# Kernel tuning notes

Measured on AMD Instinct MI355X. Metric: run time of the kernel, lower is better.

Reference implementation:

```python
import math
import jax, jax.numpy as jnp
import numpy as np

THETA = 10000.0

def _rope_rotate(x, pos):
    # x: [N,H,T,d] with d even; pos: [T] (int or float positions)
    d = x.shape[-1]
    freqs = THETA ** (-jnp.arange(0, d, 2, dtype=jnp.float32) / d)      # [d/2]
    ang = pos.astype(jnp.float32)[:, None] * freqs                       # [T, d/2]
    cos, sin = jnp.cos(ang), jnp.sin(ang)                                # broadcast over N,H
    x1, x2 = x[..., 0::2], x[..., 1::2]                                  # interleaved pairs
    r1 = x1 * cos - x2 * sin
    r2 = x1 * sin + x2 * cos
    return jnp.stack([r1, r2], axis=-1).reshape(x.shape)

def _apply_rope_2d(q, k, pos_h, pos_w):
    # axial 2D RoPE: first half of head_dim rotated by pos_h, second half by pos_w
    dh = q.shape[-1]
    half = dh // 2
    q = jnp.concatenate([_rope_rotate(q[..., :half], pos_h),
                         _rope_rotate(q[..., half:], pos_w)], axis=-1)
    k = jnp.concatenate([_rope_rotate(k[..., :half], pos_h),
                         _rope_rotate(k[..., half:], pos_w)], axis=-1)
    return q, k

def setup_inputs() -> dict:
    key = jax.random.key(0)
    ks = jax.random.split(key, 6)
    N, T, D, H = 4, 2048, 512, 8
    GH, GW = 64, 32  # 64x32 token grid, GH*GW == T
    x = jax.random.normal(ks[0], (N, T, D), dtype=jnp.float32)
    idx = jnp.arange(T, dtype=jnp.int32)
    pos_h = idx // GW
    pos_w = idx % GW
    scale_in = 1.0 / math.sqrt(D)
    w_qkv = jax.random.normal(ks[1], (D, 3 * D), dtype=jnp.float32) * scale_in
    w_proj = jax.random.normal(ks[2], (D, D), dtype=jnp.float32) * scale_in
    b_proj = jnp.zeros((D,), dtype=jnp.float32)
    return {"x": x, "pos_h": pos_h, "pos_w": pos_w,
            "w_qkv": w_qkv, "w_proj": w_proj, "b_proj": b_proj}

def reference(x, pos_h, pos_w, w_qkv, w_proj, b_proj):
    N, T, D = x.shape
    H = 8
    Dh = D // H
    qkv = x @ w_qkv                                   # [N,T,3D]
    q, k, v = jnp.split(qkv, 3, axis=-1)
    def to_heads(t):
        return t.reshape(N, T, H, Dh).transpose(0, 2, 1, 3)  # [N,H,T,Dh]
    q, k, v = to_heads(q), to_heads(k), to_heads(v)
    q, k = _apply_rope_2d(q, k, pos_h, pos_w)
    attn = jnp.einsum('nhtd,nhsd->nhts', q, k) * (1.0 / math.sqrt(Dh))  # [N,H,T,T]
    p = jax.nn.softmax(attn, axis=-1)
    o = jnp.einsum('nhts,nhsd->nhtd', p, v)           # [N,H,T,Dh]
    o = o.transpose(0, 2, 1, 3).reshape(N, T, D)
    return o @ w_proj + b_proj
```

## Files before the change

kernel.cpp:

```cpp
#include <hip/hip_runtime.h>

typedef __attribute__((ext_vector_type(4))) float f32x4;
typedef __attribute__((ext_vector_type(8))) _Float16 f16x8;
typedef __attribute__((ext_vector_type(2))) __fp16 fp16x2_raw;
typedef __attribute__((ext_vector_type(4))) unsigned int u32x4;
typedef __attribute__((ext_vector_type(2))) unsigned int u32x2;

#define MFMA_F16(a, b, c) __builtin_amdgcn_mfma_f32_16x16x32_f16((a), (b), (c), 0, 0, 0)

__device__ __forceinline__ unsigned int pkrtz(float a, float b) {
  union { fp16x2_raw h; unsigned int u; } v;
  v.h = __builtin_amdgcn_cvt_pkrtz(a, b);
  return v.u;
}

__device__ __forceinline__ float fexp2(float x) {
#if __has_builtin(__builtin_amdgcn_exp2f)
  return __builtin_amdgcn_exp2f(x);
#else
  float r;
  asm("v_exp_f32 %0, %1" : "=v"(r) : "v"(x));
  return r;
#endif
}
__device__ __forceinline__ float fsin_rev(float x) {
#if __has_builtin(__builtin_amdgcn_sinf)
  return __builtin_amdgcn_sinf(x);
#else
  float r; asm("v_sin_f32 %0, %1" : "=v"(r) : "v"(x)); return r;
#endif
}
__device__ __forceinline__ float fcos_rev(float x) {
#if __has_builtin(__builtin_amdgcn_cosf)
  return __builtin_amdgcn_cosf(x);
#else
  float r; asm("v_cos_f32 %0, %1" : "=v"(r) : "v"(x)); return r;
#endif
}

typedef const __attribute__((address_space(1))) unsigned int ga_u32_t;
typedef __attribute__((address_space(3))) unsigned int ls_u32_t;
__device__ __forceinline__ void gload16(const void* g, void* l) {
  __builtin_amdgcn_global_load_lds((ga_u32_t*)g, (ls_u32_t*)l, 16, 0, 0);
}

__device__ __forceinline__ void inv_swz64(int seg, int lane, int& r, int& ch) {
  int r_hi = seg * 8 + (lane >> 3);
  int r0 = ((lane >> 2) & 1) ^ ((r_hi >> 1) & 1);
  r = (r_hi << 1) | r0;
  ch = (lane & 3) ^ (r & 3);
}

__global__ __launch_bounds__(256)
void k_prep(const float* __restrict__ x, _Float16* __restrict__ xh,
            const float* __restrict__ wq, _Float16* __restrict__ wqT,
            const float* __restrict__ wp, _Float16* __restrict__ wpT) {
  const int b = blockIdx.x;
  const int tid = threadIdx.x;
  if (b < 4096) {
    int i = (b * 256 + tid) * 4;
    f32x4 v = *(const f32x4*)(x + i);
    u32x2 p;
    p.x = pkrtz(v[0], v[1]);
    p.y = pkrtz(v[2], v[3]);
    *(u32x2*)(xh + i) = p;
    return;
  }
  __shared__ float t[64][65];
  const int wb = b - 4096;
  const int bx = wb & 31, by = wb >> 5;
  const float* in = (bx < 24) ? wq : wp;
  _Float16* out = (bx < 24) ? wqT : wpT;
  const int N = (bx < 24) ? 1536 : 512;
  const int bn = ((bx < 24) ? bx : bx - 24) * 64, bk = by * 64;
  #pragma unroll
  for (int it = 0; it < 16; ++it) {
    int idx = it * 256 + tid;
    int kk = idx >> 6, nn = idx & 63;
    t[kk][nn] = in[(bk + kk) * N + bn + nn];
  }
  __syncthreads();
  #pragma unroll
  for (int it = 0; it < 16; ++it) {
    int idx = it * 256 + tid;
    int nn = idx >> 6, kk = idx & 63;
    out[(bn + nn) * 512 + bk + kk] = (_Float16)t[kk][nn];
  }
}

__global__ __launch_bounds__(256, 3)
void k_gemm_qkv(const _Float16* __restrict__ xh,
                const _Float16* __restrict__ wT,
                const int* __restrict__ pos_h,
                const int* __restrict__ pos_w,
                _Float16* __restrict__ qh,
                _Float16* __restrict__ kh,
                _Float16* __restrict__ vT) {
  __shared__ char As[8192], Bs[8192];
  const int tid = threadIdx.x;
  const int lane = tid & 63, w = tid >> 6;
  const int lr = lane & 15, g = lane >> 4;
  const int m0 = blockIdx.y * 128;
  const int n0 = blockIdx.x * 128;
  const int wr = w >> 1, wc = w & 1;

  const _Float16* asrc[2];
  const _Float16* bsrc[2];
  #pragma unroll
  for (int c = 0; c < 2; ++c) {
    int seg = w * 2 + c, r, ch;
    inv_swz64(seg, lane, r, ch);
    asrc[c] = xh + (size_t)(m0 + r) * 512 + ch * 8;
    bsrc[c] = wT + (size_t)(n0 + r) * 512 + ch * 8;
  }

  f32x4 acc[4][4];
  #pragma unroll
  for (int i = 0; i < 4; ++i)
    #pragma unroll
    for (int j = 0; j < 4; ++j) acc[i][j] = (f32x4){0.f, 0.f, 0.f, 0.f};

  for (int kt = 0; kt < 16; ++kt) {
    const int k0 = kt * 32;
    __syncthreads();
    #pragma unroll
    for (int c = 0; c < 2; ++c) {
      gload16(asrc[c] + k0, As + (w * 2 + c) * 1024);
      gload16(bsrc[c] + k0, Bs + (w * 2 + c) * 1024);
    }
    __syncthreads();

    f16x8 af[4], bf[4];
    #pragma unroll
    for (int mi = 0; mi < 4; ++mi) {
      int r = 64 * wr + 16 * mi + lr;
      af[mi] = *(const f16x8*)(As + (((r << 6) + (g << 4)) ^ ((r & 7) << 4)));
    }
    #pragma unroll
    for (int nj = 0; nj < 4; ++nj) {
      int r = 64 * wc + 16 * nj + lr;
      bf[nj] = *(const f16x8*)(Bs + (((r << 6) + (g << 4)) ^ ((r & 7) << 4)));
    }
    __builtin_amdgcn_s_setprio(1);
    #pragma unroll
    for (int mi = 0; mi < 4; ++mi)
      #pragma unroll
      for (int nj = 0; nj < 4; ++nj)
        acc[mi][nj] = MFMA_F16(af[mi], bf[nj], acc[mi][nj]);
    __builtin_amdgcn_s_setprio(0);
  }

  #pragma unroll
  for (int mi = 0; mi < 4; ++mi) {
    const int r0f = m0 + 64 * wr + 16 * mi + 4 * g;
    const int n = r0f >> 11;
    const int t = r0f & 2047;
    #pragma unroll
    for (int nj = 0; nj < 4; ++nj) {
      const int c = n0 + 64 * wc + 16 * nj + lr;
      const int mat = c >> 9;
      const int hh = (c >> 6) & 7;
      const int dh = c & 63;
      f32x4 v = acc[mi][nj];
      if (mat == 2) {
        int tperm = (t & ~31) + 8 * ((t >> 2) & 3) + 4 * ((t >> 4) & 1);
        u32x2 pk2;
        pk2.x = pkrtz(v[0], v[1]);
        pk2.y = pkrtz(v[2], v[3]);
        *(u32x2*)(vT + (size_t)((n * 8 + hh) * 64 + dh) * 2048 + tperm) = pk2;
      } else {
        const int p = (dh & 31) >> 1;
        const float freq_rev = fexp2((float)p * -0.8304820237218405f) * 0.15915494309189535f;
        const int odd = lane & 1;
        const int* posArr = (dh < 32) ? pos_h : pos_w;
        _Float16* dst = mat ? kh : qh;
        const float scale = mat ? 1.0f : 0.125f * 1.44269504088896f;
        #pragma unroll
        for (int i = 0; i < 4; ++i) {
          float val = v[i];
          float oth = __shfl_xor(val, 1);
          float ar = (float)posArr[t + i] * freq_rev;
          ar = ar - floorf(ar);
          float sv = fsin_rev(ar);
          float cv = fcos_rev(ar);
          float x1 = odd ? oth : val;
          float x2 = odd ? val : oth;
          float res = odd ? (x1 * sv + x2 * cv) : (x1 * cv - x2 * sv);
          dst[(size_t)((n * 8 + hh) * 2048 + t + i) * 64 + dh] = (_Float16)(res * scale);
        }
      }
    }
  }
}

__global__ __launch_bounds__(256, 3)
void k_attn(const _Float16* __restrict__ qh,
            const _Float16* __restrict__ kh,
            const _Float16* __restrict__ vp,
            _Float16* __restrict__ o_flat) {
  __shared__ char Ks[2][16384];
  __shared__ char Vs[16384];
  const int tid = threadIdx.x, lane = tid & 63, w = tid >> 6;
  const int lr = lane & 15, g = lane >> 4;
  const int bid = blockIdx.x;
  const int qt = (bid >> 3) & 15;
  const int nh = (bid & 7) + 8 * (bid >> 7);

  f16x8 qf[2][2];
  const _Float16* qbase = qh + ((size_t)nh * 2048 + qt * 128 + w * 32) * 64;
  #pragma unroll
  for (int mi = 0; mi < 2; ++mi)
    #pragma unroll
    for (int kg = 0; kg < 2; ++kg)
      qf[mi][kg] = *(const f16x8*)(qbase + (16 * mi + lr) * 64 + kg * 32 + g * 8);

  f16x8 ones;
  #pragma unroll
  for (int i = 0; i < 8; ++i) ones[i] = (_Float16)1.0f;

  f32x4 oacc[2][4];
  f32x4 lacc4[2];
  #pragma unroll
  for (int mi = 0; mi < 2; ++mi) {
    lacc4[mi] = (f32x4){0.f, 0.f, 0.f, 0.f};
    #pragma unroll
    for (int nf = 0; nf < 4; ++nf) oacc[mi][nf] = (f32x4){0.f, 0.f, 0.f, 0.f};
  }

  const _Float16* kb = kh + (size_t)nh * 2048 * 64;
  const _Float16* vb = vp + (size_t)nh * 64 * 2048;

  const int rr = lane >> 3, cc = lane & 7;
  const _Float16* ksrc[2];
  const _Float16* vsrc[2];
  #pragma unroll
  for (int c = 0; c < 2; ++c) {
    int seg = w * 2 + c;
    int r = seg * 8 + rr;
    ksrc[c] = kb + (size_t)r * 64 + ((cc ^ (r & 7)) << 3);
    vsrc[c] = vb + (size_t)r * 2048 + ((cc ^ (r & 7)) << 3);
  }
  auto stageK = [&](int b, int kt2) {
    #pragma unroll
    for (int h = 0; h < 2; ++h) {
      int kt = kt2 * 2 + h;
      #pragma unroll
      for (int c = 0; c < 2; ++c)
        gload16(ksrc[c] + (size_t)kt * 4096, Ks[b] + h * 8192 + (w * 2 + c) * 1024);
    }
  };
  auto stageV = [&](int kt2) {
    #pragma unroll
    for (int h = 0; h < 2; ++h) {
      int kt = kt2 * 2 + h;
      #pragma unroll
      for (int c = 0; c < 2; ++c)
        gload16(vsrc[c] + (size_t)kt * 64, Vs + h * 8192 + (w * 2 + c) * 1024);
    }
  };

  stageK(0, 0);

  const f32x4 cinit = (f32x4){-8.f, -8.f, -8.f, -8.f};

  for (int kt2 = 0; kt2 < 16; ++kt2) {
    const int cur = kt2 & 1;
    asm volatile("" ::: "memory");
    __builtin_amdgcn_s_barrier();
    stageV(kt2);
    if (kt2 + 1 < 16) {
      stageK(cur ^ 1, kt2 + 1);
      asm volatile("s_waitcnt vmcnt(4)" ::: "memory");
    } else {
      asm volatile("s_waitcnt vmcnt(0)" ::: "memory");
    }
    __builtin_amdgcn_s_barrier();
    asm volatile("" ::: "memory");

    f32x4 sacc[2][2][4];
    #pragma unroll
    for (int h = 0; h < 2; ++h)
      #pragma unroll
      for (int mi = 0; mi < 2; ++mi)
        #pragma unroll
        for (int sj = 0; sj < 4; ++sj) sacc[h][mi][sj] = cinit;

    __builtin_amdgcn_s_setprio(1);
    #pragma unroll
    for (int h = 0; h < 2; ++h) {
      const char* Kb = Ks[cur] + h * 8192;
      #pragma unroll
      for (int sj = 0; sj < 4; ++sj) {
        int s = sj * 16 + lr;
        int rb = s << 7, sw = (s & 7) << 4;
        #pragma unroll
        for (int kg = 0; kg < 2; ++kg) {
          f16x8 kf = *(const f16x8*)(Kb + ((rb + (kg << 6) + (g << 4)) ^ sw));
          sacc[h][0][sj] = MFMA_F16(kf, qf[0][kg], sacc[h][0][sj]);
          sacc[h][1][sj] = MFMA_F16(kf, qf[1][kg], sacc[h][1][sj]);
        }
      }
    }
    __builtin_amdgcn_s_setprio(0);

    #pragma unroll
    for (int h = 0; h < 2; ++h) {
      const char* Vb = Vs + h * 8192;
      #pragma unroll
      for (int mi = 0; mi < 2; ++mi)
        #pragma unroll
        for (int sj = 0; sj < 4; ++sj) {
          sacc[h][mi][sj][0] = fexp2(sacc[h][mi][sj][0]);
          sacc[h][mi][sj][1] = fexp2(sacc[h][mi][sj][1]);
          sacc[h][mi][sj][2] = fexp2(sacc[h][mi][sj][2]);
          sacc[h][mi][sj][3] = fexp2(sacc[h][mi][sj][3]);
        }
      __builtin_amdgcn_s_setprio(1);
      #pragma unroll
      for (int t = 0; t < 2; ++t) {
        f16x8 vf[4];
        #pragma unroll
        for (int nf = 0; nf < 4; ++nf) {
          int dh = 16 * nf + lr;
          vf[nf] = *(const f16x8*)(Vb + (((dh << 7) + (t << 6) + (g << 4)) ^ ((dh & 7) << 4)));
        }
        #pragma unroll
        for (int mi = 0; mi < 2; ++mi) {
          union { unsigned int u[4]; f16x8 h; } pb;
          pb.u[0] = pkrtz(sacc[h][mi][2 * t][0], sacc[h][mi][2 * t][1]);
          pb.u[1] = pkrtz(sacc[h][mi][2 * t][2], sacc[h][mi][2 * t][3]);
          pb.u[2] = pkrtz(sacc[h][mi][2 * t + 1][0], sacc[h][mi][2 * t + 1][1]);
          pb.u[3] = pkrtz(sacc[h][mi][2 * t + 1][2], sacc[h][mi][2 * t + 1][3]);
          lacc4[mi] = MFMA_F16(ones, pb.h, lacc4[mi]);
          #pragma unroll
          for (int nf = 0; nf < 4; ++nf)
            oacc[mi][nf] = MFMA_F16(vf[nf], pb.h, oacc[mi][nf]);
        }
      }
      __builtin_amdgcn_s_setprio(0);
    }
  }

  const int n = nh >> 3, h2 = nh & 7;
  #pragma unroll
  for (int mi = 0; mi < 2; ++mi) {
    float inv = 1.0f / lacc4[mi][0];
    int row = qt * 128 + w * 32 + 16 * mi + lr;
    _Float16* orow = o_flat + ((size_t)(n * 2048 + row)) * 512 + h2 * 64;
    #pragma unroll
    for (int nf = 0; nf < 4; ++nf) {
      u32x2 pk2;
      pk2.x = pkrtz(oacc[mi][nf][0] * inv, oacc[mi][nf][1] * inv);
      pk2.y = pkrtz(oacc[mi][nf][2] * inv, oacc[mi][nf][3] * inv);
      *(u32x2*)(orow + 16 * nf + 4 * g) = pk2;
    }
  }
}

__global__ __launch_bounds__(256, 3)
void k_gemm_proj(const _Float16* __restrict__ o_flat,
                 const _Float16* __restrict__ wpT,
                 const float* __restrict__ bias,
                 float* __restrict__ out) {
  __shared__ char As[8192], Bs[8192];
  const int tid = threadIdx.x;
  const int lane = tid & 63, w = tid >> 6;
  const int lr = lane & 15, g = lane >> 4;
  const int m0 = blockIdx.y * 128;
  const int n0 = blockIdx.x * 128;
  const int wr = w >> 1, wc = w & 1;

  const _Float16* asrc[2];
  const _Float16* bsrc[2];
  #pragma unroll
  for (int c = 0; c < 2; ++c) {
    int seg = w * 2 + c, r, ch;
    inv_swz64(seg, lane, r, ch);
    asrc[c] = o_flat + (size_t)(m0 + r) * 512 + ch * 8;
    bsrc[c] = wpT + (size_t)(n0 + r) * 512 + ch * 8;
  }

  f32x4 acc[4][4];
  #pragma unroll
  for (int i = 0; i < 4; ++i)
    #pragma unroll
    for (int j = 0; j < 4; ++j) acc[i][j] = (f32x4){0.f, 0.f, 0.f, 0.f};

  for (int kt = 0; kt < 16; ++kt) {
    const int k0 = kt * 32;
    __syncthreads();
    #pragma unroll
    for (int c = 0; c < 2; ++c) {
      gload16(asrc[c] + k0, As + (w * 2 + c) * 1024);
      gload16(bsrc[c] + k0, Bs + (w * 2 + c) * 1024);
    }
    __syncthreads();

    f16x8 af[4], bf[4];
    #pragma unroll
    for (int mi = 0; mi < 4; ++mi) {
      int r = 64 * wr + 16 * mi + lr;
      af[mi] = *(const f16x8*)(As + (((r << 6) + (g << 4)) ^ ((r & 7) << 4)));
    }
    #pragma unroll
    for (int nj = 0; nj < 4; ++nj) {
      int r = 64 * wc + 16 * nj + lr;
      bf[nj] = *(const f16x8*)(Bs + (((r << 6) + (g << 4)) ^ ((r & 7) << 4)));
    }
    __builtin_amdgcn_s_setprio(1);
    #pragma unroll
    for (int mi = 0; mi < 4; ++mi)
      #pragma unroll
      for (int nj = 0; nj < 4; ++nj)
        acc[mi][nj] = MFMA_F16(af[mi], bf[nj], acc[mi][nj]);
    __builtin_amdgcn_s_setprio(0);
  }

  #pragma unroll
  for (int mi = 0; mi < 4; ++mi) {
    int r0f = m0 + 64 * wr + 16 * mi + 4 * g;
    #pragma unroll
    for (int nj = 0; nj < 4; ++nj) {
      int c = n0 + 64 * wc + 16 * nj + lr;
      float b = bias[c];
      #pragma unroll
      for (int i = 0; i < 4; ++i)
        out[(size_t)(r0f + i) * 512 + c] = acc[mi][nj][i] + b;
    }
  }
}

extern "C" void kernel_launch(void* const* d_in, const int* in_sizes, int n_in,
                              void* d_out, int out_size, void* d_ws, size_t ws_size,
                              hipStream_t stream) {
  const float* x      = (const float*)d_in[0];
  const int*   pos_h  = (const int*)d_in[1];
  const int*   pos_w  = (const int*)d_in[2];
  const float* w_qkv  = (const float*)d_in[3];
  const float* w_proj = (const float*)d_in[4];
  const float* b_proj = (const float*)d_in[5];
  float* out = (float*)d_out;

  char* ws = (char*)d_ws;
  size_t off = 0;
  auto alloc = [&](size_t bytes) {
    char* p = ws + off;
    off += (bytes + 1023) & ~(size_t)1023;
    return p;
  };
  _Float16* xh     = (_Float16*)alloc((size_t)8192 * 512 * 2);
  _Float16* qh     = (_Float16*)alloc((size_t)32 * 2048 * 64 * 2);
  _Float16* kh     = (_Float16*)alloc((size_t)32 * 2048 * 64 * 2);
  _Float16* vT     = (_Float16*)alloc((size_t)32 * 2048 * 64 * 2);
  _Float16* o_flat = (_Float16*)alloc((size_t)8192 * 512 * 2);
  _Float16* wqT    = (_Float16*)alloc((size_t)1536 * 512 * 2);
  _Float16* wpT    = (_Float16*)alloc((size_t)512 * 512 * 2);

  hipLaunchKernelGGL(k_prep, dim3(4352), dim3(256), 0, stream,
                     x, xh, w_qkv, wqT, w_proj, wpT);
  hipLaunchKernelGGL(k_gemm_qkv, dim3(12, 64), dim3(256), 0, stream,
                     xh, wqT, pos_h, pos_w, qh, kh, vT);
  hipLaunchKernelGGL(k_attn, dim3(512), dim3(256), 0, stream, qh, kh, vT, o_flat);
  hipLaunchKernelGGL(k_gemm_proj, dim3(4, 64), dim3(256), 0, stream, o_flat, wpT, b_proj, out);
}
```

Baseline: 89.59 us.

## Split attention KV range in two and combine partial outputs

Splits each attention block's key/value sweep into two halves, doubling the grid from 512 to 1024 blocks. Each half writes an unnormalized fp16 partial output and its row sum, and a new combine kernel adds the two and normalizes into o_flat. This works because the softmax uses a fixed max offset (-8), so no rescaling between halves is needed. The aim is better occupancy and load balance across the CUs, at the cost of an extra launch, extra global traffic for the partials, and fp16 rounding of unnormalized partial sums.

```diff
diff --git a/kernel.cpp b/kernel.cpp
--- a/kernel.cpp
+++ b/kernel.cpp
@@ -197,14 +197,16 @@
 void k_attn(const _Float16* __restrict__ qh,
             const _Float16* __restrict__ kh,
             const _Float16* __restrict__ vp,
-            _Float16* __restrict__ o_flat) {
+            _Float16* __restrict__ opart,
+            float* __restrict__ ml) {
   __shared__ char Ks[2][16384];
   __shared__ char Vs[16384];
   const int tid = threadIdx.x, lane = tid & 63, w = tid >> 6;
   const int lr = lane & 15, g = lane >> 4;
   const int bid = blockIdx.x;
-  const int qt = (bid >> 3) & 15;
-  const int nh = (bid & 7) + 8 * (bid >> 7);
+  const int sp = (bid >> 3) & 1;
+  const int qt = (bid >> 4) & 15;
+  const int nh = (bid & 7) + 8 * (bid >> 8);
 
   f16x8 qf[2][2];
   const _Float16* qbase = qh + ((size_t)nh * 2048 + qt * 128 + w * 32) * 64;
@@ -259,17 +261,18 @@
     }
   };
 
-  stageK(0, 0);
+  const int kt0 = sp * 8;
+  stageK(0, kt0);
 
   const f32x4 cinit = (f32x4){-8.f, -8.f, -8.f, -8.f};
 
-  for (int kt2 = 0; kt2 < 16; ++kt2) {
-    const int cur = kt2 & 1;
+  for (int k2 = 0; k2 < 8; ++k2) {
+    const int cur = k2 & 1;
     asm volatile("" ::: "memory");
     __builtin_amdgcn_s_barrier();
-    stageV(kt2);
-    if (kt2 + 1 < 16) {
-      stageK(cur ^ 1, kt2 + 1);
+    stageV(kt0 + k2);
+    if (k2 + 1 < 8) {
+      stageK(cur ^ 1, kt0 + k2 + 1);
       asm volatile("s_waitcnt vmcnt(4)" ::: "memory");
     } else {
       asm volatile("s_waitcnt vmcnt(0)" ::: "memory");
@@ -341,20 +344,41 @@
     }
   }
 
-  const int n = nh >> 3, h2 = nh & 7;
+  const int ridb = nh * 2048 + qt * 128 + w * 32;
   #pragma unroll
   for (int mi = 0; mi < 2; ++mi) {
-    float inv = 1.0f / lacc4[mi][0];
-    int row = qt * 128 + w * 32 + 16 * mi + lr;
-    _Float16* orow = o_flat + ((size_t)(n * 2048 + row)) * 512 + h2 * 64;
+    const int rid = ridb + 16 * mi + lr;
+    _Float16* orow = opart + ((size_t)sp * 65536 + rid) * 64;
     #pragma unroll
     for (int nf = 0; nf < 4; ++nf) {
       u32x2 pk2;
-      pk2.x = pkrtz(oacc[mi][nf][0] * inv, oacc[mi][nf][1] * inv);
-      pk2.y = pkrtz(oacc[mi][nf][2] * inv, oacc[mi][nf][3] * inv);
+      pk2.x = pkrtz(oacc[mi][nf][0], oacc[mi][nf][1]);
+      pk2.y = pkrtz(oacc[mi][nf][2], oacc[mi][nf][3]);
       *(u32x2*)(orow + 16 * nf + 4 * g) = pk2;
     }
-  }
+    if (g == 0) ml[(size_t)sp * 65536 + rid] = lacc4[mi][0];
+  }
+}
+
+__global__ __launch_bounds__(256)
+void k_combine(const _Float16* __restrict__ opart,
+               const float* __restrict__ ml,
+               _Float16* __restrict__ o_flat) {
+  int t = blockIdx.x * 256 + threadIdx.x;
+  int rid = t >> 3, c8 = (t & 7) * 8;
+  float inv = 1.0f / (ml[rid] + ml[65536 + rid]);
+  union { u32x4 u; _Float16 h[8]; } o0, o1, r;
+  o0.u = *(const u32x4*)(opart + (size_t)rid * 64 + c8);
+  o1.u = *(const u32x4*)(opart + ((size_t)65536 + rid) * 64 + c8);
+  #pragma unroll
+  for (int i = 0; i < 4; ++i) {
+    float lo = ((float)o0.h[2 * i]     + (float)o1.h[2 * i]) * inv;
+    float hi = ((float)o0.h[2 * i + 1] + (float)o1.h[2 * i + 1]) * inv;
+    ((unsigned int*)&r.u)[i] = pkrtz(lo, hi);
+  }
+  int nh = rid >> 11, row = rid & 2047;
+  int n = nh >> 3, h = nh & 7;
+  *(u32x4*)(o_flat + (size_t)(n * 2048 + row) * 512 + h * 64 + c8) = r.u;
 }
 
 __global__ __launch_bounds__(256, 3)
@@ -455,11 +479,14 @@
   _Float16* o_flat = (_Float16*)alloc((size_t)8192 * 512 * 2);
   _Float16* wqT    = (_Float16*)alloc((size_t)1536 * 512 * 2);
   _Float16* wpT    = (_Float16*)alloc((size_t)512 * 512 * 2);
+  _Float16* opart  = (_Float16*)alloc((size_t)2 * 65536 * 64 * 2);
+  float*    ml     = (float*)alloc((size_t)2 * 65536 * 4);
 
   hipLaunchKernelGGL(k_prep, dim3(4352), dim3(256), 0, stream,
                      x, xh, w_qkv, wqT, w_proj, wpT);
   hipLaunchKernelGGL(k_gemm_qkv, dim3(12, 64), dim3(256), 0, stream,
                      xh, wqT, pos_h, pos_w, qh, kh, vT);
-  hipLaunchKernelGGL(k_attn, dim3(512), dim3(256), 0, stream, qh, kh, vT, o_flat);
+  hipLaunchKernelGGL(k_attn, dim3(1024), dim3(256), 0, stream, qh, kh, vT, opart, ml);
+  hipLaunchKernelGGL(k_combine, dim3(2048), dim3(256), 0, stream, opart, ml, o_flat);
   hipLaunchKernelGGL(k_gemm_proj, dim3(4, 64), dim3(256), 0, stream, o_flat, wpT, b_proj, out);
 }
```

Result: slower. 96.88 us (+8.1%).
